# Optimization experiments

Measured on AMD Instinct MI355X. Metric: run time of the kernel, lower is better.

Reference implementation:

```python
import jax, jax.numpy as jnp
import numpy as np

B, K, D, V = 8192, 32, 128, 2048
WEIGHT, SIGMA, NDCG_K = 0.15, 1.0, 10
N = K + 1


def _to_hyperboloid(x):
    # lift spatial coords onto Lorentz hyperboloid: x0 = sqrt(1 + ||x||^2)
    t = jnp.sqrt(1.0 + jnp.sum(x * x, axis=-1, keepdims=True))
    return jnp.concatenate([t, x], axis=-1)


def _lorentz_dist(u, v):
    # d(u,v) = arccosh(-<u,v>_L), <u,v>_L = -u0*v0 + u[1:].v[1:]
    inner = -u[..., 0] * v[..., 0] + jnp.sum(u[..., 1:] * v[..., 1:], axis=-1)
    return jnp.arccosh(jnp.maximum(-inner, 1.0 + 1e-7))


def setup_inputs() -> dict:
    key = jax.random.key(0)
    k = jax.random.split(key, 7)
    anchor_emb = _to_hyperboloid(jax.random.normal(k[0], (B, D), dtype=jnp.float32))
    positive_emb = _to_hyperboloid(jax.random.normal(k[1], (B, D), dtype=jnp.float32))
    negative_embs = _to_hyperboloid(jax.random.normal(k[2], (B * K, D), dtype=jnp.float32))
    tree_distances = jax.random.uniform(k[3], (V, V), dtype=jnp.float32) * 10.0
    anchor_idx = jax.random.randint(k[4], (B,), 0, V, dtype=jnp.int32)
    pos_idx = jax.random.randint(k[5], (B,), 0, V, dtype=jnp.int32)
    neg_idx = jax.random.randint(k[6], (B, K), 0, V, dtype=jnp.int32)
    return {"anchor_emb": anchor_emb, "positive_emb": positive_emb,
            "negative_embs": negative_embs, "tree_distances": tree_distances,
            "anchor_idx": anchor_idx, "pos_idx": pos_idx, "neg_idx": neg_idx}


def _lambdarank(anchor_emb, positive_emb, negative_embs, tree_distances,
                anchor_idx, pos_idx, neg_idx):
    neg = negative_embs.reshape(B, K, -1)
    pos_dist = _lorentz_dist(anchor_emb, positive_emb)            # (B,)
    neg_dists = _lorentz_dist(anchor_emb[:, None, :], neg)        # (B,K)
    d = jnp.concatenate([pos_dist[:, None], neg_dists], axis=1)   # (B,N)

    pos_t = tree_distances[anchor_idx, pos_idx]                   # (B,)
    neg_t = tree_distances[anchor_idx[:, None], neg_idx]          # (B,K)
    t = jnp.concatenate([pos_t[:, None], neg_t], axis=1)          # (B,N)
    max_t = jnp.max(t, axis=1, keepdims=True)
    rel = (max_t - t + 1e-6) / (max_t + 1e-6)                     # (B,N)

    k_top = min(NDCG_K, N)
    # 1-based rank of each item under ascending-distance sort (piecewise const)
    ranks = jnp.argsort(jnp.argsort(d, axis=1), axis=1) + 1       # (B,N)
    disc = jnp.where(ranks <= k_top,
                     1.0 / jnp.log2(ranks.astype(jnp.float32) + 1.0), 0.0)
    ideal = -jnp.sort(-rel, axis=1)[:, :k_top]                    # (B,k)
    log_pos = jnp.log2(jnp.arange(2, k_top + 2, dtype=jnp.float32))
    idcg = jnp.sum(ideal / log_pos, axis=1)                       # (B,)

    # closed-form |delta NDCG| of swapping items i,j in the ranking:
    # |(rel_i - rel_j) * (disc_i - disc_j)| / IDCG
    drel = rel[:, :, None] - rel[:, None, :]                      # (B,N,N)
    ddisc = disc[:, :, None] - disc[:, None, :]
    inv_idcg = jnp.where(idcg > 0, 1.0 / idcg, 0.0)[:, None, None]
    delta = jnp.abs(drel * ddisc) * inv_idcg

    # lambda_ij = sign(rel_i-rel_j) * delta * sigmoid(sign * sigma * (d_j - d_i))
    S = jnp.sign(drel)
    dd = d[:, None, :] - d[:, :, None]                            # d_j - d_i
    lam = S * delta * jax.nn.sigmoid(S * SIGMA * dd)
    # loss = sum_{i<j} lam_ij*(d_i-d_j); antisymmetric -> 0.5 * full sum
    loss_b = 0.5 * jnp.sum(lam * (-dd), axis=(1, 2))              # (B,)
    return WEIGHT * jnp.mean(loss_b)


def reference(anchor_emb, positive_emb, negative_embs, tree_distances,
              anchor_idx, pos_idx, neg_idx):
    return _lambdarank(anchor_emb, positive_emb, negative_embs, tree_distances,
                       anchor_idx, pos_idx, neg_idx)
```

## Files before the change

### kernel.cpp

```cpp
#include <hip/hip_runtime.h>
#include <math.h>

#define BB 8192
#define KK 32
#define DD 129
#define VV 2048
#define NN 33
#define TOPK 10

__global__ __launch_bounds__(256) void lr_main(
    const float* __restrict__ anchor,
    const float* __restrict__ positive,
    const float* __restrict__ neg,
    const float* __restrict__ tree,
    const int* __restrict__ a_idx,
    const int* __restrict__ p_idx,
    const int* __restrict__ n_idx,
    float* __restrict__ partial)
{
    __shared__ float sA[DD];
    __shared__ float sP[DD];
    __shared__ float sR[KK * DD];
    __shared__ float sd[NN];
    __shared__ float st_[NN];
    __shared__ float srel[NN];
    __shared__ float sdisc[NN];
    __shared__ float sidcg[NN];
    __shared__ float sinv;
    __shared__ float swave[4];

    const int b = blockIdx.x;
    const int t = threadIdx.x;

    {
        const float4* g4 = (const float4*)(neg + (size_t)b * (KK * DD));
        float4* s4 = (float4*)sR;
        for (int i = t; i < (KK * DD) / 4; i += 256) s4[i] = g4[i];
    }
    for (int i = t; i < DD; i += 256) {
        sA[i] = anchor[(size_t)b * DD + i];
        sP[i] = positive[(size_t)b * DD + i];
    }
    if (t < NN) {
        int ai = a_idx[b];
        st_[t] = (t == 0)
            ? tree[(size_t)ai * VV + p_idx[b]]
            : tree[(size_t)ai * VV + n_idx[(size_t)b * KK + (t - 1)]];
    }
    __syncthreads();

    {
        const int wave = t >> 6;
        const int lane = t & 63;
        for (int row = wave; row < NN; row += 4) {
            const float* r = (row == 0) ? sP : (sR + (row - 1) * DD);
            float p = sA[lane] * r[lane] + sA[lane + 64] * r[lane + 64];
            if (lane == 0) p += sA[128] * r[128];
            #pragma unroll
            for (int off = 32; off > 0; off >>= 1)
                p += __shfl_xor(p, off, 64);
            if (lane == 0) {
                float x = fmaxf(2.0f * sA[0] * r[0] - p, 1.0f + 1e-07f);
                sd[row] = acoshf(x);
            }
        }
    }
    __syncthreads();

    if (t < NN) {
        float maxt = st_[0];
        #pragma unroll
        for (int j = 1; j < NN; ++j) maxt = fmaxf(maxt, st_[j]);
        srel[t] = (maxt - st_[t] + 1e-06f) / (maxt + 1e-06f);

        float di = sd[t];
        int cnt = 0;
        #pragma unroll
        for (int j = 0; j < NN; ++j) {
            float dj = sd[j];
            cnt += (int)((dj < di) | ((dj == di) & (j < t)));
        }
        int rank = cnt + 1;
        sdisc[t] = (rank <= TOPK) ? 1.0f / log2f((float)rank + 1.0f) : 0.0f;
    }
    __syncthreads();

    if (t < NN) {
        float ri = srel[t];
        int pos = 0;
        #pragma unroll
        for (int j = 0; j < NN; ++j) {
            float rj = srel[j];
            pos += (int)((rj > ri) | ((rj == ri) & (j < t)));
        }
        sidcg[t] = (pos < TOPK) ? ri / log2f((float)pos + 2.0f) : 0.0f;
    }
    __syncthreads();
    if (t == 0) {
        float idcg = 0.0f;
        #pragma unroll
        for (int j = 0; j < NN; ++j) idcg += sidcg[j];
        sinv = (idcg > 0.0f) ? 1.0f / idcg : 0.0f;
    }
    __syncthreads();

    float acc = 0.0f;
    {
        const float inv_idcg = sinv;
        for (int p = t; p < NN * NN; p += 256) {
            int i = p / NN;
            int j = p - i * NN;
            float drel  = srel[i] - srel[j];
            float ddisc = sdisc[i] - sdisc[j];
            float dd    = sd[j] - sd[i];
            float S     = (drel > 0.0f) ? 1.0f : ((drel < 0.0f) ? -1.0f : 0.0f);
            float delta = fabsf(drel * ddisc) * inv_idcg;
            float sig   = 1.0f / (1.0f + __expf(-(S * dd)));
            acc += S * delta * sig * (-dd);
        }
    }
    #pragma unroll
    for (int off = 32; off > 0; off >>= 1)
        acc += __shfl_xor(acc, off, 64);
    if ((t & 63) == 0) swave[t >> 6] = acc;
    __syncthreads();
    if (t == 0)
        partial[b] = 0.5f * (swave[0] + swave[1] + swave[2] + swave[3]);
}

__global__ __launch_bounds__(256) void lr_reduce(
    const float* __restrict__ partial, float* __restrict__ out)
{
    __shared__ float swave[4];
    float acc = 0.0f;
    for (int i = threadIdx.x; i < BB; i += 256) acc += partial[i];
    #pragma unroll
    for (int off = 32; off > 0; off >>= 1)
        acc += __shfl_xor(acc, off, 64);
    if ((threadIdx.x & 63) == 0) swave[threadIdx.x >> 6] = acc;
    __syncthreads();
    if (threadIdx.x == 0)
        out[0] = 0.15f * (swave[0] + swave[1] + swave[2] + swave[3]) * (1.0f / (float)BB);
}

extern "C" void kernel_launch(void* const* d_in, const int* in_sizes, int n_in,
                              void* d_out, int out_size, void* d_ws, size_t ws_size,
                              hipStream_t stream)
{
    const float* anchor   = (const float*)d_in[0];
    const float* positive = (const float*)d_in[1];
    const float* neg      = (const float*)d_in[2];
    const float* tree     = (const float*)d_in[3];
    const int*   a_idx    = (const int*)d_in[4];
    const int*   p_idx    = (const int*)d_in[5];
    const int*   n_idx    = (const int*)d_in[6];
    float* partial = (float*)d_ws;

    lr_main<<<BB, 256, 0, stream>>>(anchor, positive, neg, tree,
                                    a_idx, p_idx, n_idx, partial);
    lr_reduce<<<1, 256, 0, stream>>>(partial, (float*)d_out);
}
```

Baseline: 262.0 us.

## Drop LDS staging, read rows directly, fuse reduction via atomicAdd

Negative and positive rows are no longer staged in shared memory. Each 16-lane group computes one row's dot product straight from global memory, with the anchor held in registers, and the result needs only a short shuffle reduction. Per-item data is packed into a float4, the IDCG sum becomes a wave shuffle, divisions become hardware reciprocals, and acosh becomes a log/sqrt form. The separate reduce kernel is replaced by a memset plus one atomicAdd per block, which makes the summation order nondeterministic and adds a little rounding from the reciprocals.

```diff
diff --git a/kernel.cpp b/kernel.cpp
--- a/kernel.cpp
+++ b/kernel.cpp
@@ -8,7 +8,9 @@
 #define NN 33
 #define TOPK 10
 
-__global__ __launch_bounds__(256) void lr_main(
+__device__ __forceinline__ float fast_rcp(float x) { return __builtin_amdgcn_rcpf(x); }
+
+__global__ __launch_bounds__(256) void lr_fused(
     const float* __restrict__ anchor,
     const float* __restrict__ positive,
     const float* __restrict__ neg,
@@ -16,52 +18,51 @@
     const int* __restrict__ a_idx,
     const int* __restrict__ p_idx,
     const int* __restrict__ n_idx,
-    float* __restrict__ partial)
+    float* __restrict__ out)
 {
-    __shared__ float sA[DD];
-    __shared__ float sP[DD];
-    __shared__ float sR[KK * DD];
-    __shared__ float sd[NN];
-    __shared__ float st_[NN];
-    __shared__ float srel[NN];
-    __shared__ float sdisc[NN];
-    __shared__ float sidcg[NN];
-    __shared__ float sinv;
-    __shared__ float swave[4];
+    __shared__ float  st_[NN];
+    __shared__ float  sd[NN];
+    __shared__ float4 sitem[NN];
+    __shared__ float  sinv;
+    __shared__ float  swave[4];
 
-    const int b = blockIdx.x;
-    const int t = threadIdx.x;
+    const int b    = blockIdx.x;
+    const int t    = threadIdx.x;
+    const int wave = t >> 6;
+    const int lane = t & 63;
+    const int g    = lane >> 4;
+    const int subl = lane & 15;
 
-    {
-        const float4* g4 = (const float4*)(neg + (size_t)b * (KK * DD));
-        float4* s4 = (float4*)sR;
-        for (int i = t; i < (KK * DD) / 4; i += 256) s4[i] = g4[i];
-    }
-    for (int i = t; i < DD; i += 256) {
-        sA[i] = anchor[(size_t)b * DD + i];
-        sP[i] = positive[(size_t)b * DD + i];
-    }
     if (t < NN) {
         int ai = a_idx[b];
         st_[t] = (t == 0)
             ? tree[(size_t)ai * VV + p_idx[b]]
             : tree[(size_t)ai * VV + n_idx[(size_t)b * KK + (t - 1)]];
     }
-    __syncthreads();
 
-    {
-        const int wave = t >> 6;
-        const int lane = t & 63;
-        for (int row = wave; row < NN; row += 4) {
-            const float* r = (row == 0) ? sP : (sR + (row - 1) * DD);
-            float p = sA[lane] * r[lane] + sA[lane + 64] * r[lane + 64];
-            if (lane == 0) p += sA[128] * r[128];
+    const float* abase = anchor + (size_t)b * DD;
+    float areg[8];
+    #pragma unroll
+    for (int e = 0; e < 8; ++e) areg[e] = abase[e * 16 + subl];
+
+    #pragma unroll
+    for (int round = 0; round < 3; ++round) {
+        int row = round * 16 + wave * 4 + g;
+        if (row < NN) {
+            const float* r = (row == 0)
+                ? (positive + (size_t)b * DD)
+                : (neg + (size_t)b * (KK * DD) + (size_t)(row - 1) * DD);
+            float s = 0.0f;
             #pragma unroll
-            for (int off = 32; off > 0; off >>= 1)
-                p += __shfl_xor(p, off, 64);
-            if (lane == 0) {
-                float x = fmaxf(2.0f * sA[0] * r[0] - p, 1.0f + 1e-07f);
-                sd[row] = acoshf(x);
+            for (int e = 0; e < 8; ++e) s = fmaf(areg[e], r[e * 16 + subl], s);
+            s += __shfl_xor(s, 8, 64);
+            s += __shfl_xor(s, 4, 64);
+            s += __shfl_xor(s, 2, 64);
+            s += __shfl_xor(s, 1, 64);
+            if (subl == 0) {
+                float full = s + abase[128] * r[128];
+                float x = fmaxf(2.0f * areg[0] * r[0] - full, 1.0f + 1e-07f);
+                sd[row] = __logf(x + sqrtf(x * x - 1.0f));
             }
         }
     }
@@ -71,7 +72,7 @@
         float maxt = st_[0];
         #pragma unroll
         for (int j = 1; j < NN; ++j) maxt = fmaxf(maxt, st_[j]);
-        srel[t] = (maxt - st_[t] + 1e-06f) / (maxt + 1e-06f);
+        float rel = (maxt - st_[t] + 1e-06f) * fast_rcp(maxt + 1e-06f);
 
         float di = sd[t];
         int cnt = 0;
@@ -81,66 +82,55 @@
             cnt += (int)((dj < di) | ((dj == di) & (j < t)));
         }
         int rank = cnt + 1;
-        sdisc[t] = (rank <= TOPK) ? 1.0f / log2f((float)rank + 1.0f) : 0.0f;
+        float disc = (rank <= TOPK) ? fast_rcp(log2f((float)(rank + 1))) : 0.0f;
+        sitem[t] = make_float4(di, rel, disc, 0.0f);
     }
     __syncthreads();
 
-    if (t < NN) {
-        float ri = srel[t];
-        int pos = 0;
+    if (wave == 0) {
+        float c = 0.0f;
+        if (t < NN) {
+            float ri = sitem[t].y;
+            int pos = 0;
+            #pragma unroll
+            for (int j = 0; j < NN; ++j) {
+                float rj = sitem[j].y;
+                pos += (int)((rj > ri) | ((rj == ri) & (j < t)));
+            }
+            if (pos < TOPK) c = ri * fast_rcp(log2f((float)(pos + 2)));
+        }
         #pragma unroll
-        for (int j = 0; j < NN; ++j) {
-            float rj = srel[j];
-            pos += (int)((rj > ri) | ((rj == ri) & (j < t)));
-        }
-        sidcg[t] = (pos < TOPK) ? ri / log2f((float)pos + 2.0f) : 0.0f;
-    }
-    __syncthreads();
-    if (t == 0) {
-        float idcg = 0.0f;
-        #pragma unroll
-        for (int j = 0; j < NN; ++j) idcg += sidcg[j];
-        sinv = (idcg > 0.0f) ? 1.0f / idcg : 0.0f;
+        for (int off = 32; off > 0; off >>= 1) c += __shfl_xor(c, off, 64);
+        if (t == 0) sinv = (c > 0.0f) ? fast_rcp(c) : 0.0f;
     }
     __syncthreads();
 
     float acc = 0.0f;
     {
-        const float inv_idcg = sinv;
+        const float inv = sinv;
         for (int p = t; p < NN * NN; p += 256) {
             int i = p / NN;
             int j = p - i * NN;
-            float drel  = srel[i] - srel[j];
-            float ddisc = sdisc[i] - sdisc[j];
-            float dd    = sd[j] - sd[i];
-            float S     = (drel > 0.0f) ? 1.0f : ((drel < 0.0f) ? -1.0f : 0.0f);
-            float delta = fabsf(drel * ddisc) * inv_idcg;
-            float sig   = 1.0f / (1.0f + __expf(-(S * dd)));
-            acc += S * delta * sig * (-dd);
+            float4 Ii = sitem[i];
+            float4 Ij = sitem[j];
+            float dd    = Ij.x - Ii.x;
+            float drel  = Ii.y - Ij.y;
+            float ddisc = Ii.z - Ij.z;
+            float t1  = drel * fabsf(ddisc) * inv;
+            float e   = __expf(-dd);
+            float num = (drel >= 0.0f) ? 1.0f : e;
+            acc = fmaf(t1 * num * fast_rcp(1.0f + e), -dd, acc);
         }
     }
     #pragma unroll
-    for (int off = 32; off > 0; off >>= 1)
-        acc += __shfl_xor(acc, off, 64);
-    if ((t & 63) == 0) swave[t >> 6] = acc;
+    for (int off = 32; off > 0; off >>= 1) acc += __shfl_xor(acc, off, 64);
+    if (lane == 0) swave[wave] = acc;
     __syncthreads();
-    if (t == 0)
-        partial[b] = 0.5f * (swave[0] + swave[1] + swave[2] + swave[3]);
-}
-
-__global__ __launch_bounds__(256) void lr_reduce(
-    const float* __restrict__ partial, float* __restrict__ out)
-{
-    __shared__ float swave[4];
-    float acc = 0.0f;
-    for (int i = threadIdx.x; i < BB; i += 256) acc += partial[i];
-    #pragma unroll
-    for (int off = 32; off > 0; off >>= 1)
-        acc += __shfl_xor(acc, off, 64);
-    if ((threadIdx.x & 63) == 0) swave[threadIdx.x >> 6] = acc;
-    __syncthreads();
-    if (threadIdx.x == 0)
-        out[0] = 0.15f * (swave[0] + swave[1] + swave[2] + swave[3]) * (1.0f / (float)BB);
+    if (t == 0) {
+        float v = (swave[0] + swave[1] + swave[2] + swave[3])
+                  * (0.5f * 0.15f / (float)BB);
+        atomicAdd(out, v);
+    }
 }
 
 extern "C" void kernel_launch(void* const* d_in, const int* in_sizes, int n_in,
@@ -154,9 +144,8 @@
     const int*   a_idx    = (const int*)d_in[4];
     const int*   p_idx    = (const int*)d_in[5];
     const int*   n_idx    = (const int*)d_in[6];
-    float* partial = (float*)d_ws;
 
-    lr_main<<<BB, 256, 0, stream>>>(anchor, positive, neg, tree,
-                                    a_idx, p_idx, n_idx, partial);
-    lr_reduce<<<1, 256, 0, stream>>>(partial, (float*)d_out);
+    hipMemsetAsync(d_out, 0, (size_t)out_size * sizeof(float), stream);
+    lr_fused<<<BB, 256, 0, stream>>>(anchor, positive, neg, tree,
+                                     a_idx, p_idx, n_idx, (float*)d_out);
 }
```

After: 300.2 us. 1.15x slower.
